# Kernel tuning notes

Hardware: AMD Instinct MI355X
Metric: run time of the kernel (lower is better)

Reference implementation:

```python
import jax, jax.numpy as jnp
import numpy as np

B, N, D_IN, D_OUT, D_EDGE = 2, 512, 128, 128, 32
NEG_SLOPE = 0.2  # GATv2 LeakyReLU default


def _glorot(k, shape):
    lim = np.sqrt(6.0 / (shape[0] + shape[1]))
    return jax.random.uniform(k, shape, jnp.float32, -lim, lim)


def setup_inputs() -> dict:
    key = jax.random.key(0)
    ks = jax.random.split(key, 8)
    return {
        "node_features": jax.random.normal(ks[0], (B, N, D_IN), jnp.float32),
        "adj": jax.random.uniform(ks[1], (B, N, N)) < 0.1,  # sparse-ish dense adjacency
        "edge_features": jax.random.normal(ks[2], (B, N, N, D_EDGE), jnp.float32),
        "mask": jnp.ones((B, N), dtype=bool),
        "W_l": _glorot(ks[3], (D_IN, D_OUT)),   # source (lin_l)
        "b_l": jnp.zeros((D_OUT,), jnp.float32),
        "W_r": _glorot(ks[4], (D_IN, D_OUT)),   # target (lin_r)
        "b_r": jnp.zeros((D_OUT,), jnp.float32),
        "W_e": _glorot(ks[5], (D_EDGE, D_OUT)), # lin_edge (no bias)
        "att": _glorot(ks[6], (1, D_OUT))[0],   # attention vector [D_OUT]
        "bias": jnp.zeros((D_OUT,), jnp.float32),
    }


def _gatv2_dense(x, adj, e, mask, W_l, b_l, W_r, b_r, W_e, att, bias):
    # add self-loops (dense GAT convention)
    adj = adj | jnp.eye(N, dtype=bool)
    x_l = x @ W_l + b_l              # [B,N,D] source transform
    x_r = x @ W_r + b_r              # [B,N,D] target transform
    e_t = e @ W_e                    # [B,N,N,D] edge transform
    # edge (j -> i): pre[b,i,j,:] = x_l[b,j] + x_r[b,i] + e_t[b,i,j]
    pre = x_l[:, None, :, :] + x_r[:, :, None, :] + e_t
    score = jnp.einsum('bijd,d->bij', jax.nn.leaky_relu(pre, NEG_SLOPE), att)
    score = jnp.where(adj, score, -jnp.inf)
    alpha = jax.nn.softmax(score, axis=-1)  # softmax over neighbors j
    out = jnp.einsum('bij,bjd->bid', alpha, x_l) + bias
    return jnp.where(mask[:, :, None], out, 0.0)


def reference(node_features, adj, edge_features, mask, W_l, b_l, W_r, b_r, W_e, att, bias):
    return jax.nn.silu(
        _gatv2_dense(node_features, adj, edge_features, mask,
                     W_l, b_l, W_r, b_r, W_e, att, bias)
    )
```

## Files before the change

### kernel.cpp

```cpp
#include <hip/hip_runtime.h>
#include <math.h>

#define BATCH 2
#define NNODE 512
#define DIN   128
#define DOUT  128
#define DE    32
#define NEG   0.2f
#define TI    8
#define TJ    64
#define TIB   4

typedef __attribute__((ext_vector_type(8))) short bf16x8;
typedef __attribute__((ext_vector_type(4))) float f32x4;

__device__ inline short f2bf(float f) {
    union { float f; unsigned u; } v; v.f = f;
    unsigned r = v.u + 0x7fffu + ((v.u >> 16) & 1u);
    return (short)(r >> 16);
}

__device__ inline unsigned cvtpk(float lo, float hi) {
    unsigned r;
    asm("v_cvt_pk_bf16_f32 %0, %1, %2" : "=v"(r) : "v"(lo), "v"(hi));
    return r;
}
typedef union { bf16x8 v; unsigned u[4]; } bfu;

__device__ inline void gload16(const void* g, void* l) {
    __builtin_amdgcn_global_load_lds(
        (const __attribute__((address_space(1))) void*)g,
        (__attribute__((address_space(3))) void*)l, 16, 0, 0);
}

template<int CTRL>
__device__ inline float dpp_add(float x) {
    const int y = __builtin_amdgcn_update_dpp(0, __float_as_int(x), CTRL, 0xF, 0xF, false);
    return x + __int_as_float(y);
}
__device__ inline float row16_sum(float x) {
    x = dpp_add<0x128>(x);
    x = dpp_add<0x124>(x);
    x = dpp_add<0x122>(x);
    x = dpp_add<0x121>(x);
    return x;
}

__global__ __launch_bounds__(256) void xlr_kernel(
    const float* __restrict__ x,  const float* __restrict__ Wl,
    const float* __restrict__ bl, const float* __restrict__ Wr,
    const float* __restrict__ br, float* __restrict__ xl,
    float* __restrict__ xr)
{
    const int r0 = blockIdx.x * 4;
    const int d  = threadIdx.x & 127;
    const int hv = threadIdx.x >> 7;
    __shared__ float xs[4][DIN];
    for (int idx = threadIdx.x; idx < 4 * DIN; idx += 256)
        xs[idx >> 7][idx & 127] = x[(size_t)r0 * DIN + idx];
    __syncthreads();
    const int ra = 2 * hv, rb = ra + 1;
    float al0 = bl[d], al1 = al0, ar0 = br[d], ar1 = ar0;
    #pragma unroll 4
    for (int k = 0; k < DIN; ++k) {
        const float wl = Wl[k * DOUT + d], wr = Wr[k * DOUT + d];
        const float xa = xs[ra][k], xb = xs[rb][k];
        al0 = fmaf(xa, wl, al0); al1 = fmaf(xb, wl, al1);
        ar0 = fmaf(xa, wr, ar0); ar1 = fmaf(xb, wr, ar1);
    }
    xl[(size_t)(r0 + ra) * DOUT + d] = al0;
    xl[(size_t)(r0 + rb) * DOUT + d] = al1;
    xr[(size_t)(r0 + ra) * DOUT + d] = ar0;
    xr[(size_t)(r0 + rb) * DOUT + d] = ar1;
}

__global__ __launch_bounds__(256, 2) void score_kernel(
    const float* __restrict__ xl, const float* __restrict__ xr,
    const float* __restrict__ e,  const float* __restrict__ We,
    const float* __restrict__ att, float* __restrict__ sc)
{
    const int bid = blockIdx.x;
    const int jT  = bid & 7;
    const int iT  = (bid >> 3) & 63;
    const int b   = bid >> 9;
    const int i0  = iT * TI, j0 = jT * TJ;
    const int t    = threadIdx.x;
    const int wave = t >> 6;
    const int lane = t & 63;
    const int col  = lane & 15;
    const int g    = lane >> 4;

    __shared__ __align__(16) float ebuf[3][TJ * DE];
    __shared__ __align__(16) short WeT_s[DOUT][DE];
    __shared__ __align__(16) float xr_s[TI][DOUT];
    __shared__ __align__(16) float att_s[DOUT];
    __shared__ __align__(16) float sc_s[TI][TJ];

    for (int idx = t; idx < DE * DOUT; idx += 256) {
        const int k = idx >> 7, d = idx & 127;
        WeT_s[d][k] = f2bf(We[idx]);
    }
    for (int idx = t; idx < TI * DOUT; idx += 256) {
        const int ii = idx >> 7, d = idx & 127;
        xr_s[ii][d] = xr[(size_t)(b * NNODE + i0 + ii) * DOUT + d];
    }
    if (t < DOUT) att_s[t] = att[t];

    f32x4 xlv4[8];
    {
        const float* xb = xl + (size_t)(b * NNODE + j0 + wave * 16 + g * 4) * DOUT + col;
        #pragma unroll
        for (int dt = 0; dt < 8; ++dt)
            #pragma unroll
            for (int r = 0; r < 4; ++r)
                xlv4[dt][r] = xb[(size_t)r * DOUT + dt * 16];
    }
    __syncthreads();

    bf16x8 bf[8];
    float  atv[8];
    #pragma unroll
    for (int dt = 0; dt < 8; ++dt) {
        bf[dt]  = *(const bf16x8*)&WeT_s[dt * 16 + col][g * 8];
        atv[dt] = att_s[dt * 16 + col];
    }

    const float* etile = e + ((size_t)(b * NNODE + i0) * NNODE + j0) * DE;
    const size_t estep = (size_t)NNODE * DE;
    const unsigned x0  = (unsigned)((wave << 11) + (lane << 4));

    auto STAGE = [&](int s, int i) {
        const char* gsrc = (const char*)(etile + (size_t)i * estep);
        #pragma unroll
        for (int c = 0; c < 2; ++c) {
            const unsigned x  = x0 + (unsigned)(c << 10);
            const unsigned sx = x ^ (((x >> 7) & 7u) << 4);
            gload16(gsrc + sx,
                    (char*)&ebuf[s][0] + (wave << 11) + (c << 10));
        }
    };

    STAGE(0, 0);
    STAGE(1, 1);
    asm volatile("s_waitcnt vmcnt(2)" ::: "memory");
    __builtin_amdgcn_s_barrier();
    __builtin_amdgcn_sched_barrier(0);

    const int      rrow = wave * 16 + col;
    const unsigned ys   = ((unsigned)(rrow * 128 + g * 32)) ^
                          (((unsigned)(rrow & 7)) << 4);

    #pragma unroll
    for (int i = 0; i < TI; ++i) {
        if (i + 2 < TI) STAGE((i + 2) % 3, i + 2);

        const char* eb = (const char*)&ebuf[i % 3][0];
        const f32x4 a0 = *(const f32x4*)(eb + ys);
        const f32x4 a1 = *(const f32x4*)(eb + (ys ^ 16u));

        bfu af;
        af.u[0] = cvtpk(a0[0], a0[1]); af.u[1] = cvtpk(a0[2], a0[3]);
        af.u[2] = cvtpk(a1[0], a1[1]); af.u[3] = cvtpk(a1[2], a1[3]);

        float part[4] = {0.f, 0.f, 0.f, 0.f};
        #pragma unroll
        for (int dt = 0; dt < 8; ++dt) {
            const f32x4 c = __builtin_amdgcn_mfma_f32_16x16x32_bf16(af.v, bf[dt], xlv4[dt], 0, 0, 0);
            const float xrv = xr_s[i][dt * 16 + col];
            #pragma unroll
            for (int r = 0; r < 4; ++r) {
                float p = c[r] + xrv;
                p = fmaxf(p, NEG * p);
                part[r] = fmaf(atv[dt], p, part[r]);
            }
        }
        #pragma unroll
        for (int r = 0; r < 4; ++r) part[r] = row16_sum(part[r]);

        if (col == 0) {
            float4 v; float* vp = (float*)&v;
            #pragma unroll
            for (int r = 0; r < 4; ++r) vp[r] = part[r];
            *(float4*)&sc_s[i][wave * 16 + g * 4] = v;
        }

        if (i < TI - 2) asm volatile("s_waitcnt vmcnt(2)" ::: "memory");
        else            asm volatile("s_waitcnt vmcnt(0)" ::: "memory");
        __builtin_amdgcn_s_barrier();
        __builtin_amdgcn_sched_barrier(0);
    }

    __syncthreads();
    if (t < (TI * TJ) / 4) {
        const int row = t >> 4, c4 = (t & 15) * 4;
        *(float4*)&sc[(size_t)(b * NNODE + i0 + row) * NNODE + j0 + c4] =
            *(const float4*)&sc_s[row][c4];
    }
}

__global__ __launch_bounds__(256) void agg_kernel(
    const float* __restrict__ xl, const float* __restrict__ sc,
    const void* __restrict__ adjv, const void* __restrict__ maskv,
    const float* __restrict__ bias, float* __restrict__ out)
{
    const int bid = blockIdx.x;
    const int dh  = bid & 1;
    const int iT  = (bid >> 1) & 127;
    const int b   = bid >> 8;
    const int i0  = iT * TIB, d0 = dh * 64;
    const int t    = threadIdx.x;
    const int wave = t >> 6;
    const int lane = t & 63;

    __shared__ float al_s[TIB][NNODE];
    __shared__ float ps_s[4][TIB][64];
    __shared__ float inv_s[TIB];
    __shared__ int   mflag[2];

    if (t < 2) mflag[t] = 0;
    {
        const unsigned* aw = (const unsigned*)adjv;
        unsigned sawF = 0, sawG = 0;
        #pragma unroll
        for (int k = 0; k < 16; ++k) {
            const unsigned w = aw[t + 256 * k];
            sawF |= (w == 0x3f800000u);
            sawG |= (w > 1u);
        }
        if (sawF) atomicOr(&mflag[0], 1);
        if (sawG) atomicOr(&mflag[1], 1);
    }
    for (int idx = t; idx < TIB * NNODE; idx += 256) {
        const int r = idx >> 9, jj = idx & 511;
        al_s[r][jj] = sc[(size_t)(b * NNODE + i0 + r) * NNODE + jj];
    }
    __syncthreads();
    const int byteMode = (!mflag[0] && mflag[1]) ? 1 : 0;

    {
        const int ig = i0 + wave;
        const unsigned char* aB = (const unsigned char*)adjv + (size_t)(b * NNODE + ig) * NNODE;
        const unsigned*      aW = (const unsigned*)adjv + (size_t)(b * NNODE + ig) * NNODE;
        float v[8], m = -1e30f;
        #pragma unroll
        for (int k = 0; k < 8; ++k) {
            const int j = lane + 64 * k;
            const bool conn = (j == ig) ||
                (byteMode ? (aB[j] != 0) : (aW[j] != 0));
            v[k] = conn ? al_s[wave][j] : -1e30f;
            m = fmaxf(m, v[k]);
        }
        #pragma unroll
        for (int off = 32; off; off >>= 1) m = fmaxf(m, __shfl_xor(m, off, 64));
        float s = 0.f;
        #pragma unroll
        for (int k = 0; k < 8; ++k) {
            const float ex = __expf(v[k] - m);
            al_s[wave][lane + 64 * k] = ex;
            s += ex;
        }
        #pragma unroll
        for (int off = 32; off; off >>= 1) s += __shfl_xor(s, off, 64);
        if (lane == 0) inv_s[wave] = 1.f / s;
    }
    __syncthreads();

    const int d = d0 + lane;
    const float* xb = xl + (size_t)b * NNODE * DOUT + d;
    float ac[TIB] = {0.f, 0.f, 0.f, 0.f};
    const int jlo = wave * 128;
    for (int j4 = jlo; j4 < jlo + 128; j4 += 4) {
        const f32x4 a0 = *(const f32x4*)&al_s[0][j4];
        const f32x4 a1 = *(const f32x4*)&al_s[1][j4];
        const f32x4 a2 = *(const f32x4*)&al_s[2][j4];
        const f32x4 a3 = *(const f32x4*)&al_s[3][j4];
        #pragma unroll
        for (int k = 0; k < 4; ++k) {
            const float xv = xb[(size_t)(j4 + k) * DOUT];
            ac[0] = fmaf(a0[k], xv, ac[0]);
            ac[1] = fmaf(a1[k], xv, ac[1]);
            ac[2] = fmaf(a2[k], xv, ac[2]);
            ac[3] = fmaf(a3[k], xv, ac[3]);
        }
    }
    #pragma unroll
    for (int r = 0; r < TIB; ++r) ps_s[wave][r][lane] = ac[r];
    __syncthreads();

    {
        const int r = wave;
        float val = (ps_s[0][r][lane] + ps_s[1][r][lane]) +
                    (ps_s[2][r][lane] + ps_s[3][r][lane]);
        const int mi = b * NNODE + i0 + r;
        const bool mv = byteMode ? (((const unsigned char*)maskv)[mi] != 0)
                                 : (((const unsigned*)maskv)[mi] != 0);
        val = val * inv_s[r] + bias[d];
        if (!mv) val = 0.f;
        val = val / (1.f + __expf(-val));
        out[(size_t)mi * DOUT + d] = val;
    }
}

extern "C" void kernel_launch(void* const* d_in, const int* in_sizes, int n_in,
                              void* d_out, int out_size, void* d_ws, size_t ws_size,
                              hipStream_t stream)
{
    const float* x    = (const float*)d_in[0];
    const void*  adj  = d_in[1];
    const float* e    = (const float*)d_in[2];
    const void*  mask = d_in[3];
    const float* Wl   = (const float*)d_in[4];
    const float* bl   = (const float*)d_in[5];
    const float* Wr   = (const float*)d_in[6];
    const float* br   = (const float*)d_in[7];
    const float* We   = (const float*)d_in[8];
    const float* att  = (const float*)d_in[9];
    const float* bias = (const float*)d_in[10];
    float*       out  = (float*)d_out;

    float* xl = (float*)d_ws;
    float* xr = xl + (size_t)BATCH * NNODE * DOUT;
    float* sc = xr + (size_t)BATCH * NNODE * DOUT;

    xlr_kernel<<<(BATCH * NNODE) / 4, 256, 0, stream>>>(x, Wl, bl, Wr, br, xl, xr);
    score_kernel<<<BATCH * (NNODE / TI) * (NNODE / TJ), 256, 0, stream>>>(
        xl, xr, e, We, att, sc);
    agg_kernel<<<BATCH * (NNODE / TIB) * 2, 256, 0, stream>>>(
        xl, sc, adj, mask, bias, out);
}
```

Measured before the change: 51.40 us.

## Prefetch all edge tiles up front and drop per-row barriers in score kernel

The 3-slot rotating LDS ring with per-iteration waitcnt and barriers is replaced by issuing global-to-LDS loads for all eight edge rows at kernel start. The We^T staging buffer is padded, and We is packed into it with the packed bf16 convert instruction. Scores are now stored straight to global memory, which removes the sc_s staging buffer and its final barrier. The goal is more loads in flight and less barrier stalling. The cost is a much larger LDS footprint (about 80KB per block), which may limit how many blocks fit on each CU.

```diff
diff --git a/kernel.cpp b/kernel.cpp
--- a/kernel.cpp
+++ b/kernel.cpp
@@ -10,6 +10,7 @@
 #define TI    8
 #define TJ    64
 #define TIB   4
+#define WEP   (DE + 8)
 
 typedef __attribute__((ext_vector_type(8))) short bf16x8;
 typedef __attribute__((ext_vector_type(4))) float f32x4;
@@ -90,15 +91,33 @@
     const int col  = lane & 15;
     const int g    = lane >> 4;
 
-    __shared__ __align__(16) float ebuf[3][TJ * DE];
-    __shared__ __align__(16) short WeT_s[DOUT][DE];
-    __shared__ __align__(16) float xr_s[TI][DOUT];
-    __shared__ __align__(16) float att_s[DOUT];
-    __shared__ __align__(16) float sc_s[TI][TJ];
-
-    for (int idx = t; idx < DE * DOUT; idx += 256) {
-        const int k = idx >> 7, d = idx & 127;
-        WeT_s[d][k] = f2bf(We[idx]);
+    __shared__ __align__(16) float ebuf[TI][TJ * DE];
+    __shared__ short WeT_s[DOUT][WEP];
+    __shared__ float xr_s[TI][DOUT];
+    __shared__ float att_s[DOUT];
+
+    {
+        const float* etile = e + ((size_t)(b * NNODE + i0) * NNODE + j0) * DE;
+        const size_t estep = (size_t)NNODE * DE;
+        const unsigned x0  = (unsigned)((wave << 11) + (lane << 4));
+        #pragma unroll
+        for (int i = 0; i < TI; ++i) {
+            const char* gsrc = (const char*)(etile + (size_t)i * estep);
+            #pragma unroll
+            for (int c = 0; c < 2; ++c) {
+                const unsigned x  = x0 + (unsigned)(c << 10);
+                const unsigned sx = x ^ (((x >> 7) & 7u) << 4);
+                gload16(gsrc + sx,
+                        (char*)&ebuf[i][0] + (wave << 11) + (c << 10));
+            }
+        }
+    }
+
+    for (int idx = t; idx < (DE / 2) * DOUT; idx += 256) {
+        const int k2 = idx >> 7, d = idx & 127;
+        const unsigned pk = cvtpk(We[(2 * k2) * DOUT + d],
+                                  We[(2 * k2 + 1) * DOUT + d]);
+        *(unsigned*)&WeT_s[d][2 * k2] = pk;
     }
     for (int idx = t; idx < TI * DOUT; idx += 256) {
         const int ii = idx >> 7, d = idx & 127;
@@ -125,36 +144,14 @@
         atv[dt] = att_s[dt * 16 + col];
     }
 
-    const float* etile = e + ((size_t)(b * NNODE + i0) * NNODE + j0) * DE;
-    const size_t estep = (size_t)NNODE * DE;
-    const unsigned x0  = (unsigned)((wave << 11) + (lane << 4));
-
-    auto STAGE = [&](int s, int i) {
-        const char* gsrc = (const char*)(etile + (size_t)i * estep);
-        #pragma unroll
-        for (int c = 0; c < 2; ++c) {
-            const unsigned x  = x0 + (unsigned)(c << 10);
-            const unsigned sx = x ^ (((x >> 7) & 7u) << 4);
-            gload16(gsrc + sx,
-                    (char*)&ebuf[s][0] + (wave << 11) + (c << 10));
-        }
-    };
-
-    STAGE(0, 0);
-    STAGE(1, 1);
-    asm volatile("s_waitcnt vmcnt(2)" ::: "memory");
-    __builtin_amdgcn_s_barrier();
-    __builtin_amdgcn_sched_barrier(0);
-
+    const int      jw   = j0 + wave * 16;
     const int      rrow = wave * 16 + col;
     const unsigned ys   = ((unsigned)(rrow * 128 + g * 32)) ^
                           (((unsigned)(rrow & 7)) << 4);
 
     #pragma unroll
     for (int i = 0; i < TI; ++i) {
-        if (i + 2 < TI) STAGE((i + 2) % 3, i + 2);
-
-        const char* eb = (const char*)&ebuf[i % 3][0];
+        const char* eb = (const char*)&ebuf[i][0];
         const f32x4 a0 = *(const f32x4*)(eb + ys);
         const f32x4 a1 = *(const f32x4*)(eb + (ys ^ 16u));
 
@@ -181,20 +178,8 @@
             float4 v; float* vp = (float*)&v;
             #pragma unroll
             for (int r = 0; r < 4; ++r) vp[r] = part[r];
-            *(float4*)&sc_s[i][wave * 16 + g * 4] = v;
-        }
-
-        if (i < TI - 2) asm volatile("s_waitcnt vmcnt(2)" ::: "memory");
-        else            asm volatile("s_waitcnt vmcnt(0)" ::: "memory");
-        __builtin_amdgcn_s_barrier();
-        __builtin_amdgcn_sched_barrier(0);
-    }
-
-    __syncthreads();
-    if (t < (TI * TJ) / 4) {
-        const int row = t >> 4, c4 = (t & 15) * 4;
-        *(float4*)&sc[(size_t)(b * NNODE + i0 + row) * NNODE + j0 + c4] =
-            *(const float4*)&sc_s[row][c4];
+            *(float4*)&sc[(size_t)(b * NNODE + i0 + i) * NNODE + jw + g * 4] = v;
+        }
     }
 }
 
```

After: 54.02 us. +5.1%, slower.
